# Performance work log

Hardware: AMD Instinct MI355X
Metric: run time of the kernel (lower is better)

Reference implementation:

```python
import jax, jax.numpy as jnp
import numpy as np

B, L, FD, G = 256, 512, 64, 32
H1, H2, DH = 512, 512, 256  # leaf_hidden=[512,512], diffuse_hidden=[256]

def _gelu(x):
    return jax.nn.gelu(x, approximate=False)  # torch nn.GELU default (erf)

def setup_inputs() -> dict:
    key = jax.random.key(0)
    ks = jax.random.split(key, 14)
    def lin(k, fan_in, shape):
        s = 1.0 / np.sqrt(fan_in)
        return jax.random.uniform(k, shape, jnp.float32, -s, s)
    return {
        "Xg": jax.random.normal(ks[0], (B, G), jnp.float32),
        "Xl": jax.random.normal(ks[1], (B, L, FD), jnp.float32),
        "W1": lin(ks[2], FD, (FD, H1)), "b1": lin(ks[3], FD, (H1,)),
        "W2": lin(ks[4], H1, (H1, H2)), "b2": lin(ks[5], H1, (H2,)),
        "wa": lin(ks[6], H2, (H2, 1)), "ba": lin(ks[7], H2, (1,)),
        "wt": lin(ks[8], H2, (H2, 1)), "bt": lin(ks[9], H2, (1,)),
        "Wd1": lin(ks[10], G + H2, (G + H2, DH)), "bd1": lin(ks[11], G + H2, (DH,)),
        "Wd2": lin(ks[12], DH, (DH, 1)), "bd2": lin(ks[13], DH, (1,)),
    }

def reference(Xg, Xl, W1, b1, W2, b2, wa, ba, wt, bt, Wd1, bd1, Wd2, bd2):
    # per-leaf MLP encoder: [B, L, FD] -> [B, L, H2]
    h = _gelu(jnp.einsum("blf,fh->blh", Xl, W1) + b1)
    h = _gelu(jnp.einsum("blh,hk->blk", h, W2) + b2)
    absorb = jax.nn.softplus(jnp.einsum("blh,ho->bl", h, wa) + ba[0])  # [B, L]
    atten = jax.nn.softplus(jnp.einsum("blh,ho->bl", h, wt) + bt[0])   # [B, L]
    # flip bottom->top to top->bottom
    absorb_tb = absorb[:, ::-1]
    atten_tb = atten[:, ::-1]
    # T_i = prod_{j<i} exp(-atten_tb_j) = exp(-exclusive_cumsum(atten_tb))
    excl = jnp.cumsum(atten_tb, axis=1) - atten_tb
    T = jnp.exp(-excl)
    captured = jnp.sum(T * absorb_tb, axis=1, keepdims=True)  # [B, 1]
    pooled = jnp.mean(h, axis=1)  # [B, H2]
    z = jnp.concatenate([Xg, pooled], axis=1)
    d = _gelu(z @ Wd1 + bd1) @ Wd2 + bd2  # [B, 1]
    return captured + d
```

## Files before the change

### kernel.cpp

```cpp
#include <hip/hip_runtime.h>
#include <hip/hip_bf16.h>
#include <math.h>

#define B_SZ   256
#define L_SZ   512
#define FD_SZ  64
#define H1_SZ  512
#define H2_SZ  512
#define G_SZ   32
#define DH_SZ  256
#define M_SZ   (B_SZ * L_SZ)

#define H1STRIDE 520

typedef __bf16 bfx8 __attribute__((ext_vector_type(8)));
typedef __bf16 bfx4 __attribute__((ext_vector_type(4)));
typedef float  f32x4 __attribute__((ext_vector_type(4)));
typedef float  f32x16 __attribute__((ext_vector_type(16)));

__device__ __forceinline__ float gelu_exact(float x) {
  return 0.5f * x * (1.0f + erff(x * 0.70710678118654752440f));
}
__device__ __forceinline__ float gelu_fast(float x) {
  float x2 = x * x;
  float w = x * fmaf(0.102943398f, x2, 2.30220931f);
  float e = __builtin_amdgcn_exp2f(-w);
  return x * __builtin_amdgcn_rcpf(1.0f + e);
}
__device__ __forceinline__ float softplus_f(float x) {
  return (x > 20.0f) ? x : log1pf(expf(x));
}
__device__ __forceinline__ __bf16 f2bf(float f) { return (__bf16)f; }

#define ROR_ADD(x, n)                                                          \
  {                                                                            \
    int _t = __builtin_amdgcn_mov_dpp(__builtin_bit_cast(int, (x)),            \
                                      0x120 + (n), 0xF, 0xF, true);            \
    (x) += __builtin_bit_cast(float, _t);                                      \
  }

#define MFMA16(a, b, c) __builtin_amdgcn_mfma_f32_16x16x32_bf16((a), (b), (c), 0, 0, 0)
#define MFMA32(a, b, c) __builtin_amdgcn_mfma_f32_32x32x16_bf16((a), (b), (c), 0, 0, 0)

__global__ void repack_kernel(const float* __restrict__ W1,
                              const float* __restrict__ W2,
                              __bf16* __restrict__ W1p,
                              __bf16* __restrict__ W2p,
                              float* __restrict__ pooled) {
  int t = blockIdx.x * 256 + threadIdx.x;
  if (t < 32768)
    *reinterpret_cast<float4*>(pooled + (size_t)t * 4) = (float4){0.f, 0.f, 0.f, 0.f};
  if (t < 4096) {
    int lane = t & 63, blk = t >> 6;
    int ks = blk & 1, mb = blk >> 1;
    int col = 16 * mb + (lane & 15);
    int kbase = ks * 32 + (lane >> 4) * 8;
    bfx8 o;
#pragma unroll
    for (int j = 0; j < 8; ++j) o[j] = f2bf(W1[(size_t)(kbase + j) * H1_SZ + col]);
    *reinterpret_cast<bfx8*>(W1p + (size_t)t * 8) = o;
  } else if (t < 4096 + 32768) {
    int t2 = t - 4096;
    int lane = t2 & 63, blk = t2 >> 6;
    int ks = blk & 31, nb = blk >> 5;
    int col = 32 * nb + (lane & 31);
    int kbase = 16 * ks + (lane >> 5) * 8;
    bfx8 o;
#pragma unroll
    for (int j = 0; j < 8; ++j) o[j] = f2bf(W2[(size_t)(kbase + j) * H2_SZ + col]);
    *reinterpret_cast<bfx8*>(W2p + (size_t)t2 * 8) = o;
  }
}

__global__ __launch_bounds__(1024, 8) void fused_kernel(
    const float* __restrict__ Xl,
    const __bf16* __restrict__ W1p, const __bf16* __restrict__ W2p,
    const float* __restrict__ b1, const float* __restrict__ b2,
    const float* __restrict__ wa, const float* __restrict__ ba,
    const float* __restrict__ wt, const float* __restrict__ bt,
    float* __restrict__ absorbW, float* __restrict__ attenW,
    float* __restrict__ pooled) {
  __shared__ __align__(16) char smem0[8192];
  __shared__ __bf16 H1s[64 * H1STRIDE];
  __bf16* Xs = reinterpret_cast<__bf16*>(smem0);
  float*  sl = reinterpret_cast<float*>(smem0);

  const int tid = threadIdx.x;
  const int lane = tid & 63;
  const int w = tid >> 6;
  const int g = lane >> 4;
  const int c = lane & 15;
  const int c32 = lane & 31;
  const int kg = lane >> 5;
  const int R0 = blockIdx.x * 64;
  const int bidx = R0 >> 9;

  {
    int idx = tid;
    int r = idx >> 4;
    int c4 = idx & 15;
    float4 v = *reinterpret_cast<const float4*>(Xl + (size_t)(R0 + r) * FD_SZ + c4 * 4);
    bfx4 bv;
    bv[0] = f2bf(v.x); bv[1] = f2bf(v.y); bv[2] = f2bf(v.z); bv[3] = f2bf(v.w);
    int chunk = c4 >> 1;
    int off = r * 64 + (((chunk ^ (r & 7)) << 3) + (c4 & 1) * 4);
    *reinterpret_cast<bfx4*>(&Xs[off]) = bv;
  }
  __syncthreads();

  f32x4 acc1[2][4];
#pragma unroll
  for (int mi = 0; mi < 2; ++mi)
#pragma unroll
    for (int ni = 0; ni < 4; ++ni) acc1[mi][ni] = (f32x4){0.f, 0.f, 0.f, 0.f};

#pragma unroll
  for (int ks = 0; ks < 2; ++ks) {
    bfx8 a1[2];
#pragma unroll
    for (int mi = 0; mi < 2; ++mi) {
      int mb = 2 * w + mi;
      a1[mi] = *reinterpret_cast<const bfx8*>(W1p + ((size_t)(mb * 2 + ks) * 64 + lane) * 8);
    }
    bfx8 bx[4];
#pragma unroll
    for (int ni = 0; ni < 4; ++ni) {
      int r = 16 * ni + c;
      int chunk = ks * 4 + g;
      bx[ni] = *reinterpret_cast<const bfx8*>(&Xs[r * 64 + ((chunk ^ (r & 7)) << 3)]);
    }
#pragma unroll
    for (int mi = 0; mi < 2; ++mi)
#pragma unroll
      for (int ni = 0; ni < 4; ++ni)
        acc1[mi][ni] = MFMA16(a1[mi], bx[ni], acc1[mi][ni]);
  }

#pragma unroll
  for (int mi = 0; mi < 2; ++mi) {
    int mb = 2 * w + mi;
    float4 bias4 = *reinterpret_cast<const float4*>(b1 + 16 * mb + 4 * g);
#pragma unroll
    for (int ni = 0; ni < 4; ++ni) {
      int r = 16 * ni + c;
      bfx4 pv;
      pv[0] = f2bf(gelu_fast(acc1[mi][ni][0] + bias4.x));
      pv[1] = f2bf(gelu_fast(acc1[mi][ni][1] + bias4.y));
      pv[2] = f2bf(gelu_fast(acc1[mi][ni][2] + bias4.z));
      pv[3] = f2bf(gelu_fast(acc1[mi][ni][3] + bias4.w));
      int off = r * H1STRIDE + 16 * mb + 4 * g;
      *reinterpret_cast<bfx4*>(&H1s[off]) = pv;
    }
  }
  __syncthreads();

  f32x16 acc2[2];
#pragma unroll
  for (int m = 0; m < 2; ++m)
#pragma unroll
    for (int q = 0; q < 16; ++q) acc2[m][q] = 0.0f;

  const __bf16* wpb = W2p + ((size_t)w * 32 * 64 + lane) * 8;
  const __bf16* h1base = &H1s[c32 * H1STRIDE + 8 * kg];
  for (int ks = 0; ks < 32; ++ks) {
    bfx8 a2[2];
#pragma unroll
    for (int m = 0; m < 2; ++m)
      a2[m] = *reinterpret_cast<const bfx8*>(h1base + m * 32 * H1STRIDE + ks * 16);
    bfx8 bw = *reinterpret_cast<const bfx8*>(wpb + (size_t)ks * 512);
    __builtin_amdgcn_s_setprio(1);
    acc2[0] = MFMA32(a2[0], bw, acc2[0]);
    acc2[1] = MFMA32(a2[1], bw, acc2[1]);
    __builtin_amdgcn_s_setprio(0);
  }

  const int col = 32 * w + c32;
  const float b2v = b2[col];
  const float wav = wa[col];
  const float wtv = wt[col];
  float pool0 = 0.0f;
  const int rbase = 4 * kg;
  const bool hi16 = (lane & 16) != 0;

#pragma unroll
  for (int m = 0; m < 2; ++m) {
#pragma unroll
    for (int q = 0; q < 8; ++q) {
      int rA = 2 * q, rB = 2 * q + 1;
      float vA = gelu_fast(acc2[m][rA] + b2v);
      float vB = gelu_fast(acc2[m][rB] + b2v);
      pool0 += vA + vB;
      float saA = vA * wav, saB = vB * wav;
      float stA = vA * wtv, stB = vB * wtv;
      float zs = hi16 ? saB : saA;
      float ys = hi16 ? saA : saB;
      float zt = hi16 ? stB : stA;
      float yt = hi16 ? stA : stB;
      ys = __shfl_xor(ys, 16, 64);
      yt = __shfl_xor(yt, 16, 64);
      float ss = zs + ys;
      float tt = zt + yt;
      ROR_ADD(ss, 8); ROR_ADD(ss, 4); ROR_ADD(ss, 2); ROR_ADD(ss, 1);
      ROR_ADD(tt, 8); ROR_ADD(tt, 4); ROR_ADD(tt, 2); ROR_ADD(tt, 1);
      if (c32 == 0) {
        int row = 32 * m + (rA & 3) + 8 * (rA >> 2) + rbase;
        *reinterpret_cast<float2*>(&sl[w * 128 + row * 2]) = make_float2(ss, tt);
      } else if (c32 == 16) {
        int row = 32 * m + (rB & 3) + 8 * (rB >> 2) + rbase;
        *reinterpret_cast<float2*>(&sl[w * 128 + row * 2]) = make_float2(ss, tt);
      }
    }
  }
  pool0 += __shfl_xor(pool0, 32, 64);
  if (lane < 32)
    atomicAdd(&pooled[bidx * H2_SZ + 32 * w + c32], pool0);
  __syncthreads();

  if (tid < 64) {
    float sa = 0.0f, st = 0.0f;
#pragma unroll
    for (int w16 = 0; w16 < 16; ++w16) {
      float2 v2 = *reinterpret_cast<float2*>(&sl[w16 * 128 + tid * 2]);
      sa += v2.x; st += v2.y;
    }
    absorbW[R0 + tid] = softplus_f(sa + ba[0]);
    attenW[R0 + tid]  = softplus_f(st + bt[0]);
  }
}

__global__ __launch_bounds__(256) void finalize_kernel(
    const float* __restrict__ Xg,
    const float* __restrict__ absorbW, const float* __restrict__ attenW,
    const float* __restrict__ pooled,
    const float* __restrict__ Wd1, const float* __restrict__ bd1,
    const float* __restrict__ Wd2, const float* __restrict__ bd2,
    float* __restrict__ out) {
  __shared__ float s0[512];
  __shared__ float s1[512];
  __shared__ float sab[512];
  __shared__ float zz[544];
  __shared__ float redc[4];
  __shared__ float redd[4];

  const int b = blockIdx.x;
  const int t = threadIdx.x;
  const int i0 = t, i1 = t + 256;

  float a0 = attenW[b * L_SZ + (L_SZ - 1 - i0)];
  float a1 = attenW[b * L_SZ + (L_SZ - 1 - i1)];
  sab[i0] = absorbW[b * L_SZ + (L_SZ - 1 - i0)];
  sab[i1] = absorbW[b * L_SZ + (L_SZ - 1 - i1)];
  s0[i0] = a0; s0[i1] = a1;
  __syncthreads();

  float* src = s0;
  float* dst = s1;
  for (int off = 1; off < 512; off <<= 1) {
    float v0 = src[i0] + ((i0 >= off) ? src[i0 - off] : 0.0f);
    float v1 = src[i1] + ((i1 >= off) ? src[i1 - off] : 0.0f);
    dst[i0] = v0; dst[i1] = v1;
    __syncthreads();
    float* tmp = src; src = dst; dst = tmp;
  }

  float p = expf(-(src[i0] - a0)) * sab[i0] + expf(-(src[i1] - a1)) * sab[i1];
#pragma unroll
  for (int off = 32; off; off >>= 1) p += __shfl_down(p, off, 64);
  if ((t & 63) == 0) redc[t >> 6] = p;

  if (t < G_SZ) zz[t] = Xg[b * G_SZ + t];
  zz[G_SZ + i0] = pooled[b * H2_SZ + i0] * (1.0f / (float)L_SZ);
  zz[G_SZ + i1] = pooled[b * H2_SZ + i1] * (1.0f / (float)L_SZ);
  __syncthreads();

  float s = bd1[t];
  for (int cc = 0; cc < G_SZ + H2_SZ; ++cc) s = fmaf(zz[cc], Wd1[cc * DH_SZ + t], s);
  float v = gelu_exact(s) * Wd2[t];
#pragma unroll
  for (int off = 32; off; off >>= 1) v += __shfl_down(v, off, 64);
  if ((t & 63) == 0) redd[t >> 6] = v;
  __syncthreads();

  if (t == 0) {
    float captured = redc[0] + redc[1] + redc[2] + redc[3];
    float d = redd[0] + redd[1] + redd[2] + redd[3] + bd2[0];
    out[b] = captured + d;
  }
}

extern "C" void kernel_launch(void* const* d_in, const int* in_sizes, int n_in,
                              void* d_out, int out_size, void* d_ws, size_t ws_size,
                              hipStream_t stream) {
  const float* Xg  = (const float*)d_in[0];
  const float* Xl  = (const float*)d_in[1];
  const float* W1  = (const float*)d_in[2];
  const float* b1  = (const float*)d_in[3];
  const float* W2  = (const float*)d_in[4];
  const float* b2  = (const float*)d_in[5];
  const float* wa  = (const float*)d_in[6];
  const float* ba  = (const float*)d_in[7];
  const float* wt  = (const float*)d_in[8];
  const float* bt  = (const float*)d_in[9];
  const float* Wd1 = (const float*)d_in[10];
  const float* bd1 = (const float*)d_in[11];
  const float* Wd2 = (const float*)d_in[12];
  const float* bd2 = (const float*)d_in[13];

  char* ws = (char*)d_ws;
  __bf16* W1p    = (__bf16*)(ws + 0);
  __bf16* W2p    = (__bf16*)(ws + 65536);
  float* absorbW = (float*)(ws + 589824);
  float* attenW  = (float*)(ws + 1114112);
  float* pooled  = (float*)(ws + 1638400);

  repack_kernel<<<144, 256, 0, stream>>>(W1, W2, W1p, W2p, pooled);
  fused_kernel<<<M_SZ / 64, 1024, 0, stream>>>(Xl, W1p, W2p, b1, b2, wa, ba,
                                               wt, bt, absorbW, attenW, pooled);
  finalize_kernel<<<B_SZ, 256, 0, stream>>>(Xg, absorbW, attenW, pooled,
                                            Wd1, bd1, Wd2, bd2, (float*)d_out);
}
```

Baseline: 140.1 us.

## Halve rows per block to 32 and software-prefetch W2 fragments

Each 1024-thread block now processes 32 rows instead of 64, so the grid doubles and LDS use per block roughly halves. This should let more blocks share a CU. The second GEMM loop now does one 32x32 MFMA per k-step instead of two, and preloads the next W2 fragment before each MFMA to hide global-load latency. The cost is that every W2 fragment is loaded from L2 twice as often overall (half the reuse per load), atomic pooled updates double, and each MFMA has less independent work to overlap.

```diff
diff --git a/kernel.cpp b/kernel.cpp
--- a/kernel.cpp
+++ b/kernel.cpp
@@ -11,6 +11,7 @@
 #define DH_SZ  256
 #define M_SZ   (B_SZ * L_SZ)
 
+#define ROWS     32
 #define H1STRIDE 520
 
 typedef __bf16 bfx8 __attribute__((ext_vector_type(8)));
@@ -80,10 +81,9 @@
     const float* __restrict__ wt, const float* __restrict__ bt,
     float* __restrict__ absorbW, float* __restrict__ attenW,
     float* __restrict__ pooled) {
-  __shared__ __align__(16) char smem0[8192];
-  __shared__ __bf16 H1s[64 * H1STRIDE];
-  __bf16* Xs = reinterpret_cast<__bf16*>(smem0);
-  float*  sl = reinterpret_cast<float*>(smem0);
+  __shared__ __bf16 Xs[ROWS * 64];
+  __shared__ __bf16 H1s[ROWS * H1STRIDE];
+  __shared__ float sl[16 * ROWS * 2];
 
   const int tid = threadIdx.x;
   const int lane = tid & 63;
@@ -92,13 +92,12 @@
   const int c = lane & 15;
   const int c32 = lane & 31;
   const int kg = lane >> 5;
-  const int R0 = blockIdx.x * 64;
+  const int R0 = blockIdx.x * ROWS;
   const int bidx = R0 >> 9;
 
-  {
-    int idx = tid;
-    int r = idx >> 4;
-    int c4 = idx & 15;
+  if (tid < 512) {
+    int r = tid >> 4;
+    int c4 = tid & 15;
     float4 v = *reinterpret_cast<const float4*>(Xl + (size_t)(R0 + r) * FD_SZ + c4 * 4);
     bfx4 bv;
     bv[0] = f2bf(v.x); bv[1] = f2bf(v.y); bv[2] = f2bf(v.z); bv[3] = f2bf(v.w);
@@ -108,11 +107,11 @@
   }
   __syncthreads();
 
-  f32x4 acc1[2][4];
+  f32x4 acc1[2][2];
 #pragma unroll
   for (int mi = 0; mi < 2; ++mi)
 #pragma unroll
-    for (int ni = 0; ni < 4; ++ni) acc1[mi][ni] = (f32x4){0.f, 0.f, 0.f, 0.f};
+    for (int ni = 0; ni < 2; ++ni) acc1[mi][ni] = (f32x4){0.f, 0.f, 0.f, 0.f};
 
 #pragma unroll
   for (int ks = 0; ks < 2; ++ks) {
@@ -122,9 +121,9 @@
       int mb = 2 * w + mi;
       a1[mi] = *reinterpret_cast<const bfx8*>(W1p + ((size_t)(mb * 2 + ks) * 64 + lane) * 8);
     }
-    bfx8 bx[4];
-#pragma unroll
-    for (int ni = 0; ni < 4; ++ni) {
+    bfx8 bx[2];
+#pragma unroll
+    for (int ni = 0; ni < 2; ++ni) {
       int r = 16 * ni + c;
       int chunk = ks * 4 + g;
       bx[ni] = *reinterpret_cast<const bfx8*>(&Xs[r * 64 + ((chunk ^ (r & 7)) << 3)]);
@@ -132,7 +131,7 @@
 #pragma unroll
     for (int mi = 0; mi < 2; ++mi)
 #pragma unroll
-      for (int ni = 0; ni < 4; ++ni)
+      for (int ni = 0; ni < 2; ++ni)
         acc1[mi][ni] = MFMA16(a1[mi], bx[ni], acc1[mi][ni]);
   }
 
@@ -141,7 +140,7 @@
     int mb = 2 * w + mi;
     float4 bias4 = *reinterpret_cast<const float4*>(b1 + 16 * mb + 4 * g);
 #pragma unroll
-    for (int ni = 0; ni < 4; ++ni) {
+    for (int ni = 0; ni < 2; ++ni) {
       int r = 16 * ni + c;
       bfx4 pv;
       pv[0] = f2bf(gelu_fast(acc1[mi][ni][0] + bias4.x));
@@ -154,24 +153,25 @@
   }
   __syncthreads();
 
-  f32x16 acc2[2];
-#pragma unroll
-  for (int m = 0; m < 2; ++m)
-#pragma unroll
-    for (int q = 0; q < 16; ++q) acc2[m][q] = 0.0f;
+  f32x16 acc2;
+#pragma unroll
+  for (int q = 0; q < 16; ++q) acc2[q] = 0.0f;
 
   const __bf16* wpb = W2p + ((size_t)w * 32 * 64 + lane) * 8;
   const __bf16* h1base = &H1s[c32 * H1STRIDE + 8 * kg];
-  for (int ks = 0; ks < 32; ++ks) {
-    bfx8 a2[2];
-#pragma unroll
-    for (int m = 0; m < 2; ++m)
-      a2[m] = *reinterpret_cast<const bfx8*>(h1base + m * 32 * H1STRIDE + ks * 16);
-    bfx8 bw = *reinterpret_cast<const bfx8*>(wpb + (size_t)ks * 512);
+  bfx8 bw = *reinterpret_cast<const bfx8*>(wpb);
+#pragma unroll 1
+  for (int ks = 0; ks < 31; ++ks) {
+    bfx8 a2 = *reinterpret_cast<const bfx8*>(h1base + ks * 16);
+    bfx8 bwn = *reinterpret_cast<const bfx8*>(wpb + (size_t)(ks + 1) * 512);
     __builtin_amdgcn_s_setprio(1);
-    acc2[0] = MFMA32(a2[0], bw, acc2[0]);
-    acc2[1] = MFMA32(a2[1], bw, acc2[1]);
+    acc2 = MFMA32(a2, bw, acc2);
     __builtin_amdgcn_s_setprio(0);
+    bw = bwn;
+  }
+  {
+    bfx8 a2 = *reinterpret_cast<const bfx8*>(h1base + 31 * 16);
+    acc2 = MFMA32(a2, bw, acc2);
   }
 
   const int col = 32 * w + c32;
@@ -183,44 +183,41 @@
   const bool hi16 = (lane & 16) != 0;
 
 #pragma unroll
-  for (int m = 0; m < 2; ++m) {
-#pragma unroll
-    for (int q = 0; q < 8; ++q) {
-      int rA = 2 * q, rB = 2 * q + 1;
-      float vA = gelu_fast(acc2[m][rA] + b2v);
-      float vB = gelu_fast(acc2[m][rB] + b2v);
-      pool0 += vA + vB;
-      float saA = vA * wav, saB = vB * wav;
-      float stA = vA * wtv, stB = vB * wtv;
-      float zs = hi16 ? saB : saA;
-      float ys = hi16 ? saA : saB;
-      float zt = hi16 ? stB : stA;
-      float yt = hi16 ? stA : stB;
-      ys = __shfl_xor(ys, 16, 64);
-      yt = __shfl_xor(yt, 16, 64);
-      float ss = zs + ys;
-      float tt = zt + yt;
-      ROR_ADD(ss, 8); ROR_ADD(ss, 4); ROR_ADD(ss, 2); ROR_ADD(ss, 1);
-      ROR_ADD(tt, 8); ROR_ADD(tt, 4); ROR_ADD(tt, 2); ROR_ADD(tt, 1);
-      if (c32 == 0) {
-        int row = 32 * m + (rA & 3) + 8 * (rA >> 2) + rbase;
-        *reinterpret_cast<float2*>(&sl[w * 128 + row * 2]) = make_float2(ss, tt);
-      } else if (c32 == 16) {
-        int row = 32 * m + (rB & 3) + 8 * (rB >> 2) + rbase;
-        *reinterpret_cast<float2*>(&sl[w * 128 + row * 2]) = make_float2(ss, tt);
-      }
+  for (int q = 0; q < 8; ++q) {
+    int rA = 2 * q, rB = 2 * q + 1;
+    float vA = gelu_fast(acc2[rA] + b2v);
+    float vB = gelu_fast(acc2[rB] + b2v);
+    pool0 += vA + vB;
+    float saA = vA * wav, saB = vB * wav;
+    float stA = vA * wtv, stB = vB * wtv;
+    float zs = hi16 ? saB : saA;
+    float ys = hi16 ? saA : saB;
+    float zt = hi16 ? stB : stA;
+    float yt = hi16 ? stA : stB;
+    ys = __shfl_xor(ys, 16, 64);
+    yt = __shfl_xor(yt, 16, 64);
+    float ss = zs + ys;
+    float tt = zt + yt;
+    ROR_ADD(ss, 8); ROR_ADD(ss, 4); ROR_ADD(ss, 2); ROR_ADD(ss, 1);
+    ROR_ADD(tt, 8); ROR_ADD(tt, 4); ROR_ADD(tt, 2); ROR_ADD(tt, 1);
+    if (c32 == 0) {
+      int row = (rA & 3) + 8 * (rA >> 2) + rbase;
+      *reinterpret_cast<float2*>(&sl[w * (2 * ROWS) + row * 2]) = make_float2(ss, tt);
+    } else if (c32 == 16) {
+      int row = (rB & 3) + 8 * (rB >> 2) + rbase;
+      *reinterpret_cast<float2*>(&sl[w * (2 * ROWS) + row * 2]) = make_float2(ss, tt);
     }
   }
   pool0 += __shfl_xor(pool0, 32, 64);
   if (lane < 32)
-    atomicAdd(&pooled[bidx * H2_SZ + 32 * w + c32], pool0);
-  __syncthreads();
-
-  if (tid < 64) {
+    atomicAdd(&pooled[bidx * H2_SZ + col], pool0);
+  __syncthreads();
+
+  if (tid < ROWS) {
     float sa = 0.0f, st = 0.0f;
 #pragma unroll
     for (int w16 = 0; w16 < 16; ++w16) {
-      float2 v2 = *reinterpret_cast<float2*>(&sl[w16 * 128 + tid * 2]);
+      float2 v2 = *reinterpret_cast<float2*>(&sl[w16 * (2 * ROWS) + tid * 2]);
       sa += v2.x; st += v2.y;
     }
     absorbW[R0 + tid] = softplus_f(sa + ba[0]);
@@ -314,8 +311,8 @@
   float* pooled  = (float*)(ws + 1638400);
 
   repack_kernel<<<144, 256, 0, stream>>>(W1, W2, W1p, W2p, pooled);
-  fused_kernel<<<M_SZ / 64, 1024, 0, stream>>>(Xl, W1p, W2p, b1, b2, wa, ba,
-                                               wt, bt, absorbW, attenW, pooled);
+  fused_kernel<<<M_SZ / ROWS, 1024, 0, stream>>>(Xl, W1p, W2p, b1, b2, wa, ba,
+                                                 wt, bt, absorbW, attenW, pooled);
   finalize_kernel<<<B_SZ, 256, 0, stream>>>(Xg, absorbW, attenW, pooled,
                                             Wd1, bd1, Wd2, bd2, (float*)d_out);
 }
```

Result: slower. 164.8 us (+17.6%).
